# Kernel tuning notes

Measured on AMD Instinct MI355X. Metric: run time of the kernel, lower is better.

Reference implementation:

```python
import jax, jax.numpy as jnp
import numpy as np

B, L, D_IN = 16, 2048, 512
HID, H = 512, 8
D = HID // H          # head dim
FACTOR = 5
U = min(FACTOR * int(np.ceil(np.log(L))), L)  # u_q == u_k == 40 (L == S)


def setup_inputs() -> dict:
    key = jax.random.key(0)
    ks = jax.random.split(key, 8)
    s = 1.0 / np.sqrt(D_IN).astype(np.float32)
    return {
        "q_in": jax.random.normal(ks[0], (B, L, D_IN), jnp.float32),
        "k_in": jax.random.normal(ks[1], (B, L, D_IN), jnp.float32),
        "v_in": jax.random.normal(ks[2], (B, L, D_IN), jnp.float32),
        "Wq": jax.random.normal(ks[3], (D_IN, HID), jnp.float32) * s,
        "Wk": jax.random.normal(ks[4], (D_IN, HID), jnp.float32) * s,
        "Wv": jax.random.normal(ks[5], (D_IN, HID), jnp.float32) * s,
        "Wo": jax.random.normal(ks[6], (HID, HID // H), jnp.float32) / np.sqrt(HID).astype(np.float32),
        "indx_q_seq": jax.random.randint(ks[7], (L,), 0, L, dtype=jnp.int32),
    }


def reference(q_in, k_in, v_in, Wq, Wk, Wv, Wo, indx_q_seq):
    # projections + (memory-reinterpreting, as in the TF source) head reshape
    q = (q_in @ Wq).reshape(B, H, L, D)
    k = (k_in @ Wk).reshape(B, H, L, D)
    v = (v_in @ Wv).reshape(B, H, L, D)

    # --- _prob_qk ---
    # TF's chained gathers on the broadcast k_expand collapse to pairing
    # query s with the single key indx_q_seq[s]; all sample_k columns of
    # Q_K_sample are identical, so M = max - sum/L = dot * (1 - U/L).
    k_sel = k[:, :, indx_q_seq, :]                        # [B,H,L,D]
    dot = jnp.einsum('bhle,bhle->bhl', q, k_sel)          # [B,H,L]
    M = dot - dot * (jnp.float32(U) / jnp.float32(L))
    _, m_top = jax.lax.top_k(M, U)                        # [B,H,U]

    b_idx = jnp.arange(B)[:, None, None]
    h_idx = jnp.arange(H)[None, :, None]
    q_red = q[b_idx, h_idx, m_top]                        # [B,H,U,D]
    scores = jnp.einsum('bhue,bhle->bhul', q_red, k)      # [B,H,U,L]
    scores = scores * (1.0 / np.sqrt(D).astype(np.float32))

    # --- initial context: causal cumsum of values ---
    context = jnp.cumsum(v, axis=-2)                      # [B,H,L,D]

    # --- update context at the top-U query positions (causal mask) ---
    causal = jnp.arange(L)[None, None, None, :] > m_top[..., None]
    scores = jnp.where(causal, -jnp.inf, scores)
    attn = jax.nn.softmax(scores, axis=-1)                # [B,H,U,L]
    upd = jnp.einsum('bhul,bhld->bhud', attn, v)          # [B,H,U,D]
    context = context.at[b_idx, h_idx, m_top].set(upd)

    out = context.reshape(B, L, HID) @ Wo                 # [B,L,HID//H]
    return out
```

## Files before the change

kernel.cpp:

```cpp
#include <hip/hip_runtime.h>
#include <hip/hip_bf16.h>
#include <math.h>

#define B_   16
#define L_   2048
#define DIN  512
#define HID_ 512
#define H_   8
#define D_   64
#define U_   40
#define BH   (B_*H_)

typedef unsigned short u16;
typedef unsigned int u32;
typedef unsigned long long u64;
typedef __bf16 bf16x8 __attribute__((ext_vector_type(8)));
typedef float f32x4 __attribute__((ext_vector_type(4)));

__device__ __forceinline__ u16 f2bf(float x) {
  __bf16 b = (__bf16)x;
  return __builtin_bit_cast(unsigned short, b);
}
__device__ __forceinline__ float bf2f(u16 h) {
  return __uint_as_float(((unsigned)h) << 16);
}
__device__ __forceinline__ u32 pk2(float a, float b) {
  return (u32)f2bf(a) | ((u32)f2bf(b) << 16);
}
__device__ __forceinline__ void gload16(const u16* g, u16* l) {
  __builtin_amdgcn_global_load_lds(
      (__attribute__((address_space(1))) void*)(g),
      (__attribute__((address_space(3))) void*)(l), 16, 0, 0);
}
__device__ __forceinline__ void gload16f(const float* g, float* l) {
  __builtin_amdgcn_global_load_lds(
      (__attribute__((address_space(1))) void*)(g),
      (__attribute__((address_space(3))) void*)(l), 16, 0, 0);
}
__device__ __forceinline__ u64 mkkey(float Mv, int l) {
  u32 fb = __float_as_uint(Mv);
  u32 mapped = (fb & 0x80000000u) ? ~fb : (fb | 0x80000000u);
  return ((u64)mapped << 32) | (u64)(0xFFFFFFFFu - (u32)l);
}

__global__ __launch_bounds__(256)
void wsplit3_kernel(const float* __restrict__ Wq, const float* __restrict__ Wk,
                    const float* __restrict__ Wv, u16* __restrict__ Bt3) {
  const float* W = (blockIdx.y == 0) ? Wq : (blockIdx.y == 1) ? Wk : Wv;
  u16* Bt = Bt3 + (size_t)blockIdx.y * 524288;
  int tid = blockIdx.x * 256 + threadIdx.x;
  int n = tid & 511, k = tid >> 9;
  float a = W[(size_t)k * 512 + n];
  u16 hi = f2bf(a);
  u16 lo = f2bf(a - bf2f(hi));
  int kb = k >> 5, kc = k & 31;
  int slotH = kc >> 3, wi = kc & 7;
  int swzH = (slotH     ^ (n & 7)) << 3;
  int swzL = ((4+slotH) ^ (n & 7)) << 3;
  Bt[(size_t)n * 1024 + kb * 64 + swzH + wi] = hi;
  Bt[(size_t)n * 1024 + kb * 64 + swzL + wi] = lo;
}

__global__ __launch_bounds__(256, 4)
void gemm_proj3(const float* __restrict__ A, const u16* __restrict__ Bt,
                float* __restrict__ C) {
  __shared__ float Asf[128 * 32];
  __shared__ u16 Bs[128 * 64];
  const int bid = blockIdx.x;
  const int g = bid >> 3;
  const int xb = (bid & 7) + ((g >> 2) << 3);
  const int yb = g & 3;
  const int t = threadIdx.x;
  const int w = t >> 6, lane = t & 63;
  const int lhi = lane >> 4, l16 = lane & 15;
  const int row0 = xb * 128, col0 = yb * 128;
  const int wrow = (w >> 1) * 64, wcol = (w & 1) * 64;

  const u16* gB = Bt + (size_t)(col0 + w * 32 + (lane >> 3)) * 1024 + (lane & 7) * 8;
  u16* lB = &Bs[(w * 32) * 64];
  const int rA0 = w * 32 + (lane >> 3);
  const int swsl = lane & 7;

  f32x4 acc[4][4];
  #pragma unroll
  for (int i = 0; i < 4; ++i)
    #pragma unroll
    for (int j = 0; j < 4; ++j) acc[i][j] = (f32x4){0.f, 0.f, 0.f, 0.f};

  for (int kb = 0; kb < 16; ++kb) {
    #pragma unroll
    for (int i = 0; i < 4; ++i)
      gload16(gB + kb * 64 + (size_t)i * 8 * 1024, lB + i * 8 * 64);
    #pragma unroll
    for (int i = 0; i < 4; ++i) {
      int r = rA0 + i * 8;
      int slot = swsl ^ (r & 7);
      gload16f(A + (size_t)(row0 + r) * 512 + kb * 32 + slot * 4,
               &Asf[(w * 32 + i * 8) * 32]);
    }
    __syncthreads();

    bf16x8 bfH[4], bfL[4];
    #pragma unroll
    for (int j = 0; j < 4; ++j) {
      int cb = wcol + j * 16 + l16;
      bfH[j] = *reinterpret_cast<const bf16x8*>(
          &Bs[cb * 64 + ((lhi ^ (cb & 7)) << 3)]);
      bfL[j] = *reinterpret_cast<const bf16x8*>(
          &Bs[cb * 64 + (((4 + lhi) ^ (cb & 7)) << 3)]);
    }
    #pragma unroll
    for (int i = 0; i < 4; ++i) {
      int ra = wrow + i * 16 + l16;
      const f32x4 x0 = *reinterpret_cast<const f32x4*>(
          &Asf[ra * 32 + (((lhi * 2)       ^ (ra & 7)) << 2)]);
      const f32x4 x1 = *reinterpret_cast<const f32x4*>(
          &Asf[ra * 32 + ((((lhi * 2) + 1) ^ (ra & 7)) << 2)]);
      bf16x8 aH;
      aH[0] = (__bf16)x0[0]; aH[1] = (__bf16)x0[1];
      aH[2] = (__bf16)x0[2]; aH[3] = (__bf16)x0[3];
      aH[4] = (__bf16)x1[0]; aH[5] = (__bf16)x1[1];
      aH[6] = (__bf16)x1[2]; aH[7] = (__bf16)x1[3];
      #pragma unroll
      for (int j = 0; j < 4; ++j)
        acc[i][j] = __builtin_amdgcn_mfma_f32_16x16x32_bf16(aH, bfH[j], acc[i][j], 0, 0, 0);
      bf16x8 aL;
      aL[0] = (__bf16)(x0[0] - (float)aH[0]); aL[1] = (__bf16)(x0[1] - (float)aH[1]);
      aL[2] = (__bf16)(x0[2] - (float)aH[2]); aL[3] = (__bf16)(x0[3] - (float)aH[3]);
      aL[4] = (__bf16)(x1[0] - (float)aH[4]); aL[5] = (__bf16)(x1[1] - (float)aH[5]);
      aL[6] = (__bf16)(x1[2] - (float)aH[6]); aL[7] = (__bf16)(x1[3] - (float)aH[7]);
      #pragma unroll
      for (int j = 0; j < 4; ++j)
        acc[i][j] = __builtin_amdgcn_mfma_f32_16x16x32_bf16(aH, bfL[j], acc[i][j], 0, 0, 0);
      #pragma unroll
      for (int j = 0; j < 4; ++j)
        acc[i][j] = __builtin_amdgcn_mfma_f32_16x16x32_bf16(aL, bfH[j], acc[i][j], 0, 0, 0);
    }
    __syncthreads();
  }
  #pragma unroll
  for (int i = 0; i < 4; ++i)
    #pragma unroll
    for (int j = 0; j < 4; ++j)
      #pragma unroll
      for (int r = 0; r < 4; ++r)
        C[(size_t)(row0 + wrow + i * 16 + lhi * 4 + r) * 512
          + col0 + wcol + j * 16 + l16] = acc[i][j][r];
}

__global__ __launch_bounds__(256, 2)
void gemm_proj_v(const float* __restrict__ A, const u16* __restrict__ Bt,
                 u16* __restrict__ C) {
  __shared__ float Asf[2][128 * 32];
  __shared__ u16 Bs[2][128 * 64];
  const int bid = blockIdx.x;
  const int g = bid >> 3;
  const int xb = (bid & 7) + ((g >> 2) << 3);
  const int yb = g & 3;
  const int t = threadIdx.x;
  const int w = t >> 6, lane = t & 63;
  const int lhi = lane >> 4, l16 = lane & 15;
  const int row0 = xb * 128, col0 = yb * 128;
  const int wrow = (w >> 1) * 64, wcol = (w & 1) * 64;

  const u16* gB = Bt + (size_t)(col0 + w * 32 + (lane >> 3)) * 1024 + (lane & 7) * 8;
  const int rA0 = w * 32 + (lane >> 3);
  const int swsl = lane & 7;

  f32x4 acc[4][4];
  #pragma unroll
  for (int i = 0; i < 4; ++i)
    #pragma unroll
    for (int j = 0; j < 4; ++j) acc[i][j] = (f32x4){0.f, 0.f, 0.f, 0.f};

#define STAGEV(KB, NB)                                                          \
  { u16* lB = &Bs[NB][(w * 32) * 64];                                           \
    _Pragma("unroll") for (int i = 0; i < 4; ++i)                               \
      gload16(gB + (KB) * 64 + (size_t)i * 8 * 1024, lB + i * 8 * 64);          \
    _Pragma("unroll") for (int i = 0; i < 4; ++i) {                             \
      int r = rA0 + i * 8;                                                      \
      int slot = swsl ^ (r & 7);                                                \
      gload16f(A + (size_t)(row0 + r) * 512 + (KB) * 32 + slot * 4,             \
               &Asf[NB][(w * 32 + i * 8) * 32]); } }

  STAGEV(0, 0)
  __syncthreads();

  for (int kb = 0; kb < 16; ++kb) {
    const int cur = kb & 1;
    if (kb < 15) STAGEV(kb + 1, cur ^ 1)
    bf16x8 bfH[4];
    #pragma unroll
    for (int j = 0; j < 4; ++j) {
      int cb = wcol + j * 16 + l16;
      bfH[j] = *reinterpret_cast<const bf16x8*>(
          &Bs[cur][cb * 64 + ((lhi ^ (cb & 7)) << 3)]);
    }
    #pragma unroll
    for (int i = 0; i < 4; ++i) {
      int ra = wrow + i * 16 + l16;
      const f32x4 x0 = *reinterpret_cast<const f32x4*>(
          &Asf[cur][ra * 32 + (((lhi * 2)       ^ (ra & 7)) << 2)]);
      const f32x4 x1 = *reinterpret_cast<const f32x4*>(
          &Asf[cur][ra * 32 + ((((lhi * 2) + 1) ^ (ra & 7)) << 2)]);
      bf16x8 aH;
      aH[0] = (__bf16)x0[0]; aH[1] = (__bf16)x0[1];
      aH[2] = (__bf16)x0[2]; aH[3] = (__bf16)x0[3];
      aH[4] = (__bf16)x1[0]; aH[5] = (__bf16)x1[1];
      aH[6] = (__bf16)x1[2]; aH[7] = (__bf16)x1[3];
      #pragma unroll
      for (int j = 0; j < 4; ++j)
        acc[i][j] = __builtin_amdgcn_mfma_f32_16x16x32_bf16(aH, bfH[j], acc[i][j], 0, 0, 0);
    }
    __syncthreads();
  }
#undef STAGEV
  #pragma unroll
  for (int i = 0; i < 4; ++i)
    #pragma unroll
    for (int j = 0; j < 4; ++j)
      #pragma unroll
      for (int r = 0; r < 4; ++r)
        C[(size_t)(row0 + wrow + i * 16 + lhi * 4 + r) * 512
          + col0 + wcol + j * 16 + l16] = f2bf(acc[i][j][r]);
}

__global__ __launch_bounds__(256)
void dotsel_kernel(const float* __restrict__ qp, const float* __restrict__ kp,
                   const int* __restrict__ indx, u64* __restrict__ cand) {
  __shared__ u64 keys[256];
  __shared__ u64 wmax[2][4];
  const int bh = blockIdx.x, ch = blockIdx.y;
  const int t = threadIdx.x, w = t >> 6, lane = t & 63;
  const size_t boff = (size_t)bh * 131072;
  const int l0 = ch * 256 + w * 64;
  const float cUL = 40.0f / 2048.0f;
  const int li = lane >> 4;
  const int dq = lane & 15;

  #pragma unroll 4
  for (int i = 0; i < 16; ++i) {
    int l = l0 + i * 4 + li;
    int ls = indx[l];
    float4 q4 = *reinterpret_cast<const float4*>(&qp[boff + (size_t)l * 64 + dq * 4]);
    float4 k4 = *reinterpret_cast<const float4*>(&kp[boff + (size_t)ls * 64 + dq * 4]);
    float p = q4.x * k4.x + q4.y * k4.y + q4.z * k4.z + q4.w * k4.w;
    p += __shfl_xor(p, 1, 64);
    p += __shfl_xor(p, 2, 64);
    p += __shfl_xor(p, 4, 64);
    p += __shfl_xor(p, 8, 64);
    if (dq == 0) {
      float Mv = p - p * cUL;
      keys[w * 64 + i * 4 + li] = mkkey(Mv, l);
    }
  }
  __syncthreads();

  u64 myk = keys[t];
  for (int u = 0; u < U_; ++u) {
    u64 b = myk;
    #pragma unroll
    for (int off = 32; off >= 1; off >>= 1) {
      u64 v = __shfl_xor(b, off, 64);
      if (v > b) b = v;
    }
    if (lane == 0) wmax[u & 1][w] = b;
    __syncthreads();
    const u64* wm = wmax[u & 1];
    u64 m = wm[0];
    if (wm[1] > m) m = wm[1];
    if (wm[2] > m) m = wm[2];
    if (wm[3] > m) m = wm[3];
    if (myk == m) myk = 0;
    if (t == 0) cand[((size_t)(bh * 8 + ch)) * U_ + u] = m;
  }
}

__global__ __launch_bounds__(64)
void merge_topk(const u64* __restrict__ cand, int* __restrict__ mtop) {
  const int bh = blockIdx.x;
  const int lane = threadIdx.x;
  u64 c0 = cand[(size_t)bh * 320 + 0 * 64 + lane];
  u64 c1 = cand[(size_t)bh * 320 + 1 * 64 + lane];
  u64 c2 = cand[(size_t)bh * 320 + 2 * 64 + lane];
  u64 c3 = cand[(size_t)bh * 320 + 3 * 64 + lane];
  u64 c4 = cand[(size_t)bh * 320 + 4 * 64 + lane];
  for (int u = 0; u < U_; ++u) {
    u64 b = c0;
    if (c1 > b) b = c1;
    if (c2 > b) b = c2;
    if (c3 > b) b = c3;
    if (c4 > b) b = c4;
    #pragma unroll
    for (int off = 32; off >= 1; off >>= 1) {
      u64 v = __shfl_xor(b, off, 64);
      if (v > b) b = v;
    }
    if (c0 == b) c0 = 0;
    if (c1 == b) c1 = 0;
    if (c2 == b) c2 = 0;
    if (c3 == b) c3 = 0;
    if (c4 == b) c4 = 0;
    if (lane == 0) mtop[bh * U_ + u] = (int)(0xFFFFFFFFu - (u32)b);
  }
}

__global__ __launch_bounds__(256)
void gather_q_kernel(const float* __restrict__ qp, const int* __restrict__ mtop,
                     u16* __restrict__ qredbf) {
  int tid = blockIdx.x * 256 + threadIdx.x;
  int s = tid >> 6;
  int d = tid & 63;
  int bh = s / 48;
  int u = s - bh * 48;
  float val = 0.f;
  if (u < U_) {
    int m = mtop[bh * U_ + u];
    val = qp[(size_t)bh * (L_ * D_) + (size_t)m * D_ + d] * 0.125f;
  }
  qredbf[tid] = f2bf(val);
}

__global__ __launch_bounds__(256)
void attn_fused(const u16* __restrict__ qredbf, const float* __restrict__ kp,
                const u16* __restrict__ vbf, const int* __restrict__ mtop,
                float* __restrict__ partial, float* __restrict__ msums) {
  __shared__ u16 As[48 * 64];
  __shared__ u16 Bs[128 * 64];
  __shared__ u16 Ps[48 * 128];
  __shared__ int ms[48];
  __shared__ float redm[4][48];
  __shared__ float reds[4][48];
  const int bh = blockIdx.x, chk = blockIdx.y;
  const int l0 = chk * 128;
  const int t = threadIdx.x, w = t >> 6, lane = t & 63;
  const int lhi = lane >> 4, l16 = lane & 15;

  for (int e = t; e < 384; e += 256) {
    int r = e >> 3, s = e & 7;
    *reinterpret_cast<uint4*>(&As[r * 64 + ((s ^ (r & 7)) << 3)]) =
        *reinterpret_cast<const uint4*>(&qredbf[(size_t)bh * 3072 + e * 8]);
  }
  #pragma unroll
  for (int ee = 0; ee < 4; ++ee) {
    int e = t + ee * 256;
    int r = e >> 3, s = e & 7;
    const float* src = &kp[(size_t)bh * 131072 + (size_t)(l0 + r) * 64 + s * 8];
    float4 va = *reinterpret_cast<const float4*>(src);
    float4 vb = *reinterpret_cast<const float4*>(src + 4);
    uint4 w4 = make_uint4(pk2(va.x, va.y), pk2(va.z, va.w),
                          pk2(vb.x, vb.y), pk2(vb.z, vb.w));
    *reinterpret_cast<uint4*>(&Bs[r * 64 + ((s ^ (r & 7)) << 3)]) = w4;
  }
  if (t < 48) ms[t] = (t < U_) ? mtop[bh * U_ + t] : -1;
  __syncthreads();

  f32x4 acc[3][2];
  #pragma unroll
  for (int m = 0; m < 3; ++m)
    #pragma unroll
    for (int n = 0; n < 2; ++n) acc[m][n] = (f32x4){0.f, 0.f, 0.f, 0.f};
  #pragma unroll
  for (int ks = 0; ks < 2; ++ks) {
    bf16x8 a[3], b[2];
    #pragma unroll
    for (int m = 0; m < 3; ++m) {
      int r = m * 16 + l16;
      a[m] = *reinterpret_cast<const bf16x8*>(
          &As[r * 64 + (((ks * 4 + lhi) ^ (r & 7)) << 3)]);
    }
    #pragma unroll
    for (int n = 0; n < 2; ++n) {
      int cb = w * 32 + n * 16 + l16;
      b[n] = *reinterpret_cast<const bf16x8*>(
          &Bs[cb * 64 + (((ks * 4 + lhi) ^ (cb & 7)) << 3)]);
    }
    #pragma unroll
    for (int m = 0; m < 3; ++m)
      #pragma unroll
      for (int n = 0; n < 2; ++n)
        acc[m][n] = __builtin_amdgcn_mfma_f32_16x16x32_bf16(a[m], b[n], acc[m][n], 0, 0, 0);
  }

  float val[3][2][4], mx[3][4];
  #pragma unroll
  for (int m = 0; m < 3; ++m)
    #pragma unroll
    for (int r = 0; r < 4; ++r) {
      int u = m * 16 + lhi * 4 + r;
      float v0 = acc[m][0][r], v1 = acc[m][1][r];
      if (l0 + w * 32 + 0 * 16 + l16 > ms[u]) v0 = -INFINITY;
      if (l0 + w * 32 + 1 * 16 + l16 > ms[u]) v1 = -INFINITY;
      val[m][0][r] = v0; val[m][1][r] = v1;
      mx[m][r] = fmaxf(v0, v1);
    }
  #pragma unroll
  for (int off = 1; off <= 8; off <<= 1)
    #pragma unroll
    for (int m = 0; m < 3; ++m)
      #pragma unroll
      for (int r = 0; r < 4; ++r)
        mx[m][r] = fmaxf(mx[m][r], __shfl_xor(mx[m][r], off, 64));
  if (l16 == 0) {
    #pragma unroll
    for (int m = 0; m < 3; ++m)
      #pragma unroll
      for (int r = 0; r < 4; ++r)
        redm[w][m * 16 + lhi * 4 + r] = mx[m][r];
  }
  __syncthreads();

  float sx[3][4];
  #pragma unroll
  for (int m = 0; m < 3; ++m)
    #pragma unroll
    for (int r = 0; r < 4; ++r) {
      int u = m * 16 + lhi * 4 + r;
      float mv = fmaxf(fmaxf(redm[0][u], redm[1][u]), fmaxf(redm[2][u], redm[3][u]));
      mv = (mv > -1e30f) ? mv : 0.f;
      float p0 = __expf(val[m][0][r] - mv);
      float p1 = __expf(val[m][1][r] - mv);
      sx[m][r] = p0 + p1;
      {
        int l = w * 32 + 0 * 16 + l16, s = l >> 3;
        int sw = (s & 8) | ((s & 7) ^ (u & 7));
        Ps[u * 128 + (sw << 3) + (l & 7)] = f2bf(p0);
      }
      {
        int l = w * 32 + 1 * 16 + l16, s = l >> 3;
        int sw = (s & 8) | ((s & 7) ^ (u & 7));
        Ps[u * 128 + (sw << 3) + (l & 7)] = f2bf(p1);
      }
    }
  #pragma unroll
  for (int off = 1; off <= 8; off <<= 1)
    #pragma unroll
    for (int m = 0; m < 3; ++m)
      #pragma unroll
      for (int r = 0; r < 4; ++r)
        sx[m][r] += __shfl_xor(sx[m][r], off, 64);
  if (l16 == 0) {
    #pragma unroll
    for (int m = 0; m < 3; ++m)
      #pragma unroll
      for (int r = 0; r < 4; ++r)
        reds[w][m * 16 + lhi * 4 + r] = sx[m][r];
  }
  __syncthreads();

  if (t < 48) {
    float mv = fmaxf(fmaxf(redm[0][t], redm[1][t]), fmaxf(redm[2][t], redm[3][t]));
    mv = (mv > -1e30f) ? mv : 0.f;
    float sv = reds[0][t] + reds[1][t] + reds[2][t] + reds[3][t];
    size_t o = (((size_t)chk * 128 + bh) * 48 + t) * 2;
    msums[o] = mv; msums[o + 1] = sv;
  }
  const size_t vbase = (size_t)bh * 131072;
  #pragma unroll
  for (int j = 0; j < 16; ++j) {
    int ll = w * 32 + 2 * j;
    u16 ua = vbf[vbase + (size_t)(l0 + ll) * 64 + lane];
    u16 ub = vbf[vbase + (size_t)(l0 + ll + 1) * 64 + lane];
    u32 pk = (u32)ua | ((u32)ub << 16);
    int s = ll >> 3;
    int sw = (s & 8) | ((s & 7) ^ (lane & 7));
    *reinterpret_cast<u32*>(&Bs[lane * 128 + (sw << 3) + (ll & 7)]) = pk;
  }
  __syncthreads();

  f32x4 acc2[3];
  #pragma unroll
  for (int m = 0; m < 3; ++m) acc2[m] = (f32x4){0.f, 0.f, 0.f, 0.f};
  #pragma unroll
  for (int ks = 0; ks < 4; ++ks) {
    bf16x8 b;
    { int cb = w * 16 + l16; int s = ks * 4 + lhi;
      int sw = (s & 8) | ((s & 7) ^ (cb & 7));
      b = *reinterpret_cast<const bf16x8*>(&Bs[cb * 128 + (sw << 3)]); }
    #pragma unroll
    for (int m = 0; m < 3; ++m) {
      int r = m * 16 + l16; int s = ks * 4 + lhi;
      int sw = (s & 8) | ((s & 7) ^ (r & 7));
      bf16x8 a = *reinterpret_cast<const bf16x8*>(&Ps[r * 128 + (sw << 3)]);
      acc2[m] = __builtin_amdgcn_mfma_f32_16x16x32_bf16(a, b, acc2[m], 0, 0, 0);
    }
  }
  #pragma unroll
  for (int m = 0; m < 3; ++m)
    #pragma unroll
    for (int r = 0; r < 4; ++r) {
      int u = m * 16 + lhi * 4 + r;
      partial[(((size_t)chk * 128 + bh) * 48 + u) * 64 + w * 16 + l16] = acc2[m][r];
    }
}

__global__ __launch_bounds__(256)
void merge_pv(const float* __restrict__ partial, const float* __restrict__ msums,
              float* __restrict__ upd) {
  int tid = blockIdx.x * 256 + threadIdx.x;
  int s = tid >> 6, d = tid & 63;
  int bh = s / U_, u = s - bh * U_;
  float mg = -INFINITY;
  #pragma unroll
  for (int c = 0; c < 16; ++c)
    mg = fmaxf(mg, msums[(((size_t)c * 128 + bh) * 48 + u) * 2]);
  float av = 0.f, sg = 0.f;
  #pragma unroll
  for (int c = 0; c < 16; ++c) {
    size_t o = (((size_t)c * 128 + bh) * 48 + u) * 2;
    float e = __expf(msums[o] - mg);
    av += partial[(((size_t)c * 128 + bh) * 48 + u) * 64 + d] * e;
    sg += msums[o + 1] * e;
  }
  upd[(size_t)s * 64 + d] = av / sg;
}

__global__ __launch_bounds__(256)
void cumsumA(const u16* __restrict__ vbf, float* __restrict__ seg32) {
  int bh = blockIdx.x, sg = blockIdx.y;
  int t = threadIdx.x, w = t >> 6, lane = t & 63;
  int g = sg * 4 + w;
  size_t base = (size_t)bh * 131072 + (size_t)g * 32 * 64;
  float s = 0.f;
  for (int i = 0; i < 32; ++i) s += bf2f(vbf[base + i * 64 + lane]);
  seg32[((size_t)bh * 64 + g) * 64 + lane] = s;
}
__global__ __launch_bounds__(256)
void cumsumB(const u16* __restrict__ vbf, const float* __restrict__ seg32,
             u16* __restrict__ ctxbf) {
  int bh = blockIdx.x, sg = blockIdx.y;
  int t = threadIdx.x, w = t >> 6, lane = t & 63;
  int g = sg * 4 + w;
  float run = 0.f;
  for (int s = 0; s < g; ++s) run += seg32[((size_t)bh * 64 + s) * 64 + lane];
  size_t base = (size_t)bh * 131072 + (size_t)g * 32 * 64;
  for (int i = 0; i < 32; ++i) {
    run += bf2f(vbf[base + i * 64 + lane]);
    ctxbf[base + i * 64 + lane] = f2bf(run);
  }
}

__global__ __launch_bounds__(256)
void scatter_kernel(const float* __restrict__ upd, const int* __restrict__ mtop,
                    u16* __restrict__ ctxbf) {
  int tid = blockIdx.x * 256 + threadIdx.x;
  int s = tid >> 6;
  if (s >= BH * U_) return;
  int d = tid & 63;
  int bh = s / U_;
  ctxbf[(size_t)bh * 131072 + (size_t)mtop[s] * 64 + d] = f2bf(upd[(size_t)s * 64 + d]);
}

__global__ __launch_bounds__(256)
void wo_prep(const float* __restrict__ Wo, u16* __restrict__ WoT) {
  int tid = blockIdx.x * 256 + threadIdx.x;
  int j = tid >> 9, k = tid & 511;
  float v = Wo[(size_t)k * 64 + j];
  int k0 = k & ~63, ko = k & 63;
  int ks = ko >> 5, kc = ko & 31;
  int slot = (ks * 4 + (kc >> 3)) ^ (j & 7);
  WoT[(size_t)j * 512 + k0 + (slot << 3) + (kc & 7)] = f2bf(v);
}

__global__ __launch_bounds__(256, 6)
void gemm_out(const u16* __restrict__ ctxbf, const u16* __restrict__ WoT,
              float* __restrict__ out) {
  __shared__ u16 As[64 * 64];
  __shared__ u16 Bs[64 * 64];
  const int t = threadIdx.x, w = t >> 6, lane = t & 63;
  const int lhi = lane >> 4, l16 = lane & 15;
  const int row0 = blockIdx.x * 64;
  f32x4 acc[4];
  #pragma unroll
  for (int j = 0; j < 4; ++j) acc[j] = (f32x4){0.f, 0.f, 0.f, 0.f};

  for (int k0 = 0; k0 < 512; k0 += 64) {
    #pragma unroll
    for (int ii = 0; ii < 2; ++ii) {
      int e = t + ii * 256;
      int j = e >> 3, s = e & 7;
      gload16(WoT + (size_t)j * 512 + k0 + s * 8, Bs + (size_t)(w * 64 + ii * 256) * 8);
    }
    #pragma unroll
    for (int ii = 0; ii < 2; ++ii) {
      int e = t + ii * 256;
      int r = e >> 3, s = e & 7;
      gload16(ctxbf + (size_t)(row0 + r) * 512 + k0 + (s ^ (r & 7)) * 8,
              As + (size_t)(w * 64 + ii * 256) * 8);
    }
    __syncthreads();
    #pragma unroll
    for (int ks = 0; ks < 2; ++ks) {
      int r = w * 16 + l16;
      bf16x8 a = *reinterpret_cast<const bf16x8*>(
          &As[r * 64 + (((ks * 4 + lhi) ^ (r & 7)) << 3)]);
      #pragma unroll
      for (int jf = 0; jf < 4; ++jf) {
        int cb = jf * 16 + l16;
        bf16x8 b = *reinterpret_cast<const bf16x8*>(
            &Bs[cb * 64 + (((ks * 4 + lhi) ^ (cb & 7)) << 3)]);
        acc[jf] = __builtin_amdgcn_mfma_f32_16x16x32_bf16(a, b, acc[jf], 0, 0, 0);
      }
    }
    __syncthreads();
  }
  #pragma unroll
  for (int jf = 0; jf < 4; ++jf)
    #pragma unroll
    for (int r = 0; r < 4; ++r)
      out[(size_t)(row0 + w * 16 + lhi * 4 + r) * 64 + jf * 16 + l16] = acc[jf][r];
}

extern "C" void kernel_launch(void* const* d_in, const int* in_sizes, int n_in,
                              void* d_out, int out_size, void* d_ws, size_t ws_size,
                              hipStream_t stream) {
  const float* q_in = (const float*)d_in[0];
  const float* k_in = (const float*)d_in[1];
  const float* v_in = (const float*)d_in[2];
  const float* Wq   = (const float*)d_in[3];
  const float* Wk   = (const float*)d_in[4];
  const float* Wv   = (const float*)d_in[5];
  const float* Wo   = (const float*)d_in[6];
  const int*   indx = (const int*)d_in[7];
  float* out = (float*)d_out;

  float* ws = (float*)d_ws;
  float* qp   = ws;
  float* kp   = ws + 16777216;
  u16*   vbf  = (u16*)(ws + 33554432);
  u64*   cand = (u64*)(ws + 50331648);
  u16*   WoT  = (u16*)cand;
  u16*   qredbf = (u16*)(ws + 50593792);
  int*   mtop = (int*)(ws + 50921472);
  u16*   Bt3  = (u16*)d_out;
  float* partial = qp;
  float* msums   = qp + 6291456;
  float* upd     = qp + 6488064;
  u16*   ctxbf = (u16*)kp;
  float* seg32 = kp + 8388608;

  const int M = B_ * L_;

  wsplit3_kernel<<<dim3(1024, 3), 256, 0, stream>>>(Wq, Wk, Wv, Bt3);

  gemm_proj3<<<1024, 256, 0, stream>>>(q_in, Bt3, qp);
  gemm_proj3<<<1024, 256, 0, stream>>>(k_in, Bt3 + 524288, kp);
  gemm_proj_v<<<1024, 256, 0, stream>>>(v_in, Bt3 + 1048576, vbf);

  dotsel_kernel<<<dim3(BH, 8), 256, 0, stream>>>(qp, kp, indx, cand);
  merge_topk<<<BH, 64, 0, stream>>>(cand, mtop);
  gather_q_kernel<<<(BH * 48 * 64) / 256, 256, 0, stream>>>(qp, mtop, qredbf);

  attn_fused<<<dim3(BH, 16), 256, 0, stream>>>(qredbf, kp, vbf, mtop, partial, msums);
  merge_pv<<<(BH * U_ * 64) / 256, 256, 0, stream>>>(partial, msums, upd);

  cumsumA<<<dim3(BH, 16), 256, 0, stream>>>(vbf, seg32);
  cumsumB<<<dim3(BH, 16), 256, 0, stream>>>(vbf, seg32, ctxbf);

  scatter_kernel<<<(BH * U_ * 64) / 256, 256, 0, stream>>>(upd, mtop, ctxbf);

  wo_prep<<<128, 256, 0, stream>>>(Wo, WoT);
  gemm_out<<<M / 64, 256, 0, stream>>>(ctxbf, WoT, out);
}
```

Before: 341.2 us.

## Double-buffer projection GEMM tiles and make per-chunk top-k wave-local

New measurement: 375.6 us. 10.1% more time.

```diff
diff --git a/kernel.cpp b/kernel.cpp
--- a/kernel.cpp
+++ b/kernel.cpp
@@ -61,11 +61,11 @@
   Bt[(size_t)n * 1024 + kb * 64 + swzL + wi] = lo;
 }
 
-__global__ __launch_bounds__(256, 4)
+__global__ __launch_bounds__(256, 2)
 void gemm_proj3(const float* __restrict__ A, const u16* __restrict__ Bt,
                 float* __restrict__ C) {
-  __shared__ float Asf[128 * 32];
-  __shared__ u16 Bs[128 * 64];
+  __shared__ float Asf[2][128 * 32];
+  __shared__ u16 Bs[2][128 * 64];
   const int bid = blockIdx.x;
   const int g = bid >> 3;
   const int xb = (bid & 7) + ((g >> 2) << 3);
@@ -77,7 +77,6 @@
   const int wrow = (w >> 1) * 64, wcol = (w & 1) * 64;
 
   const u16* gB = Bt + (size_t)(col0 + w * 32 + (lane >> 3)) * 1024 + (lane & 7) * 8;
-  u16* lB = &Bs[(w * 32) * 64];
   const int rA0 = w * 32 + (lane >> 3);
   const int swsl = lane & 7;
 
@@ -87,35 +86,39 @@
     #pragma unroll
     for (int j = 0; j < 4; ++j) acc[i][j] = (f32x4){0.f, 0.f, 0.f, 0.f};
 
+#define STAGE3(KB, NB)                                                          \
+  { u16* lB = &Bs[NB][(w * 32) * 64];                                           \
+    _Pragma("unroll") for (int i = 0; i < 4; ++i)                               \
+      gload16(gB + (KB) * 64 + (size_t)i * 8 * 1024, lB + i * 8 * 64);          \
+    _Pragma("unroll") for (int i = 0; i < 4; ++i) {                             \
+      int r = rA0 + i * 8;                                                      \
+      int slot = swsl ^ (r & 7);                                                \
+      gload16f(A + (size_t)(row0 + r) * 512 + (KB) * 32 + slot * 4,             \
+               &Asf[NB][(w * 32 + i * 8) * 32]); } }
+
+  STAGE3(0, 0)
+  __syncthreads();
+
   for (int kb = 0; kb < 16; ++kb) {
-    #pragma unroll
-    for (int i = 0; i < 4; ++i)
-      gload16(gB + kb * 64 + (size_t)i * 8 * 1024, lB + i * 8 * 64);
-    #pragma unroll
-    for (int i = 0; i < 4; ++i) {
-      int r = rA0 + i * 8;
-      int slot = swsl ^ (r & 7);
-      gload16f(A + (size_t)(row0 + r) * 512 + kb * 32 + slot * 4,
-               &Asf[(w * 32 + i * 8) * 32]);
-    }
-    __syncthreads();
+    const int cur = kb & 1;
+    if (kb < 15) STAGE3(kb + 1, cur ^ 1)
 
     bf16x8 bfH[4], bfL[4];
     #pragma unroll
     for (int j = 0; j < 4; ++j) {
       int cb = wcol + j * 16 + l16;
       bfH[j] = *reinterpret_cast<const bf16x8*>(
-          &Bs[cb * 64 + ((lhi ^ (cb & 7)) << 3)]);
+          &Bs[cur][cb * 64 + ((lhi ^ (cb & 7)) << 3)]);
       bfL[j] = *reinterpret_cast<const bf16x8*>(
-          &Bs[cb * 64 + (((4 + lhi) ^ (cb & 7)) << 3)]);
+          &Bs[cur][cb * 64 + (((4 + lhi) ^ (cb & 7)) << 3)]);
     }
     #pragma unroll
     for (int i = 0; i < 4; ++i) {
       int ra = wrow + i * 16 + l16;
       const f32x4 x0 = *reinterpret_cast<const f32x4*>(
-          &Asf[ra * 32 + (((lhi * 2)       ^ (ra & 7)) << 2)]);
+          &Asf[cur][ra * 32 + (((lhi * 2)       ^ (ra & 7)) << 2)]);
       const f32x4 x1 = *reinterpret_cast<const f32x4*>(
-          &Asf[ra * 32 + ((((lhi * 2) + 1) ^ (ra & 7)) << 2)]);
+          &Asf[cur][ra * 32 + ((((lhi * 2) + 1) ^ (ra & 7)) << 2)]);
       bf16x8 aH;
       aH[0] = (__bf16)x0[0]; aH[1] = (__bf16)x0[1];
       aH[2] = (__bf16)x0[2]; aH[3] = (__bf16)x0[3];
@@ -138,6 +141,7 @@
     }
     __syncthreads();
   }
+#undef STAGE3
   #pragma unroll
   for (int i = 0; i < 4; ++i)
     #pragma unroll
@@ -229,7 +233,7 @@
 void dotsel_kernel(const float* __restrict__ qp, const float* __restrict__ kp,
                    const int* __restrict__ indx, u64* __restrict__ cand) {
   __shared__ u64 keys[256];
-  __shared__ u64 wmax[2][4];
+  __shared__ u64 wl[192];
   const int bh = blockIdx.x, ch = blockIdx.y;
   const int t = threadIdx.x, w = t >> 6, lane = t & 63;
   const size_t boff = (size_t)bh * 131072;
@@ -237,6 +241,8 @@
   const float cUL = 40.0f / 2048.0f;
   const int li = lane >> 4;
   const int dq = lane & 15;
+
+  if (t >= 160 && t < 192) wl[t] = 0;
 
   #pragma unroll 4
   for (int i = 0; i < 16; ++i) {
@@ -264,15 +270,27 @@
       u64 v = __shfl_xor(b, off, 64);
       if (v > b) b = v;
     }
-    if (lane == 0) wmax[u & 1][w] = b;
-    __syncthreads();
-    const u64* wm = wmax[u & 1];
-    u64 m = wm[0];
-    if (wm[1] > m) m = wm[1];
-    if (wm[2] > m) m = wm[2];
-    if (wm[3] > m) m = wm[3];
-    if (myk == m) myk = 0;
-    if (t == 0) cand[((size_t)(bh * 8 + ch)) * U_ + u] = m;
+    if (myk == b) myk = 0;
+    if (lane == 0) wl[w * 40 + u] = b;
+  }
+  __syncthreads();
+
+  if (w == 0) {
+    u64 c0 = wl[lane], c1 = wl[64 + lane], c2 = wl[128 + lane];
+    for (int u = 0; u < U_; ++u) {
+      u64 b = c0;
+      if (c1 > b) b = c1;
+      if (c2 > b) b = c2;
+      #pragma unroll
+      for (int off = 32; off >= 1; off >>= 1) {
+        u64 v = __shfl_xor(b, off, 64);
+        if (v > b) b = v;
+      }
+      if (c0 == b) c0 = 0;
+      if (c1 == b) c1 = 0;
+      if (c2 == b) c2 = 0;
+      if (lane == 0) cand[((size_t)(bh * 8 + ch)) * U_ + u] = b;
+    }
   }
 }
 
```
